# Kernel optimization log

Hardware: AMD Instinct MI355X
Metric: run time of the kernel (lower is better)

The kernel has to match this reference:

```python
import jax, jax.numpy as jnp
import numpy as np

C = 64; H = 80; W = 120; B = 2; V = 3; BV = B * V; D = 20
NEAR = 0.1; FAR = 100.0
BF16 = jnp.bfloat16


def conv2d(x, w, b, pad):
    y = jax.lax.conv_general_dilated(x, w, (1, 1), [(pad, pad), (pad, pad)],
                                     dimension_numbers=('NCHW', 'OIHW', 'NCHW'))
    return y + b[None, :, None, None]


def bn2d(x, g, b, m, v, eps=1e-5):
    # BatchNorm2d in inference mode (running stats)
    scale = g / jnp.sqrt(v + eps)
    return (x - m[None, :, None, None]) * scale[None, :, None, None] + b[None, :, None, None]


def grid_sample(feat, grid):
    # feat [N,C,Hf,Wf], grid [N,Hg,Wg,2] in [-1,1]; bilinear, zeros padding, align_corners=True
    _, _, Hf, Wf = feat.shape
    gx = (grid[..., 0] + 1.0) * 0.5 * (Wf - 1)
    gy = (grid[..., 1] + 1.0) * 0.5 * (Hf - 1)
    x0 = jnp.floor(gx); y0 = jnp.floor(gy)

    def one(f, gx, gy, x0, y0):
        def gather(xi, yi):
            valid = (xi >= 0) & (xi < Wf) & (yi >= 0) & (yi < Hf)
            xc = jnp.clip(xi, 0, Wf - 1).astype(jnp.int32)
            yc = jnp.clip(yi, 0, Hf - 1).astype(jnp.int32)
            return f[:, yc, xc] * valid.astype(f.dtype)
        wx = gx - x0; wy = gy - y0
        return (gather(x0, y0) * ((1 - wx) * (1 - wy))
                + gather(x0 + 1, y0) * (wx * (1 - wy))
                + gather(x0, y0 + 1) * ((1 - wx) * wy)
                + gather(x0 + 1, y0 + 1) * (wx * wy))
    return jax.vmap(one)(feat, gx, gy, x0, y0)


def forward(x, intrinsics, c2ws,
            pf_bn1_g, pf_bn1_b, pf_bn1_m, pf_bn1_v, pf_w1, pf_b1,
            pf_bn2_g, pf_bn2_b, pf_bn2_m, pf_bn2_v, pf_w2, pf_b2,
            cp_w, cp_b, cf_bn_g, cf_bn_b, cf_bn_m, cf_bn_v, cf_w, cf_b):
    # ---- flag[0]: predicted depth -> world xyz, position_fusion ----
    depth = 255.0 * (0.5 * jnp.tanh(x[:, 0]) + 0.5)                       # [BV,H,W]
    d16 = depth.astype(BF16)
    ug = jnp.broadcast_to(jnp.arange(W, dtype=jnp.float32)[None, :], (H, W)).astype(BF16)
    vg = jnp.broadcast_to(jnp.arange(H, dtype=jnp.float32)[:, None], (H, W)).astype(BF16)
    cam = jnp.stack([ug[None] * d16, vg[None] * d16, d16], axis=-1).reshape(BV, H * W, 3)
    Kinv = jnp.linalg.inv(intrinsics.astype(jnp.float32)).astype(BF16)
    xyz = jnp.einsum('nij,npj->npi', Kinv, cam)                           # cam coords
    xyz = jnp.einsum('nij,npj->npi', c2ws[:, :3, :3].astype(BF16), xyz) \
          + c2ws[:, :3, 3].astype(BF16)[:, None, :]                       # world coords
    xyz = xyz.reshape(BV, H, W, 3).transpose(0, 3, 1, 2).astype(x.dtype)
    h = jnp.concatenate([xyz, x], axis=1)                                 # [BV,C+3,H,W]
    h = jax.nn.silu(conv2d(bn2d(h, pf_bn1_g, pf_bn1_b, pf_bn1_m, pf_bn1_v), pf_w1, pf_b1, 4))
    h = jax.nn.silu(conv2d(bn2d(h, pf_bn2_g, pf_bn2_b, pf_bn2_m, pf_bn2_v), pf_w2, pf_b2, 4))

    # ---- flag[1]: multi-view plane-sweep correlation ----
    xr = h.reshape(B, V, C, H, W)
    vb = lambda t: t.transpose(1, 0, 2, 3, 4).reshape(BV, C, H, W)        # 'b v ... -> (v b) ...'
    feat01 = vb(xr)
    Ki = intrinsics.reshape(B, V, 3, 3)
    intr_curr = jax.lax.stop_gradient(
        (Ki * jnp.array([W, H, 1.0], jnp.float32)[None, None, :, None]).transpose(1, 0, 2, 3).reshape(BV, 3, 3))
    E = jax.lax.stop_gradient(c2ws.reshape(B, V, 4, 4))
    Einv = jnp.linalg.inv(E)
    dmin, dmax = 1.0 / FAR, 1.0 / NEAR
    depth_vals = 1.0 / (dmin + jnp.linspace(0.0, 1.0, D) * (dmax - dmin))  # [D]
    pix = jnp.stack([jnp.broadcast_to(jnp.arange(W, dtype=jnp.float32)[None, :], (H, W)),
                     jnp.broadcast_to(jnp.arange(H, dtype=jnp.float32)[:, None], (H, W)),
                     jnp.ones((H, W), jnp.float32)], 0).reshape(3, H * W)
    Kinv_c = jnp.linalg.inv(intr_curr).astype(BF16)

    corr = 0.0
    for idx in range(1, V):
        order = list(range(V))[idx:] + list(range(V))[:idx]
        feat10 = vb(xr[:, jnp.array(order)])                              # [BV,C,H,W]
        pose = jnp.concatenate([E[:, o] @ Einv[:, v0] for v0, o in enumerate(order)], axis=0)  # [BV,4,4]
        pts = jnp.einsum('bij,jp->bip', Kinv_c, pix.astype(BF16))
        pts = jnp.einsum('bij,bjp->bip', pose[:, :3, :3].astype(BF16), pts)
        pts = pts[:, :, None, :] * depth_vals.astype(BF16)[None, None, :, None] \
              + pose[:, :3, 3].astype(BF16)[:, :, None, None]             # [BV,3,D,HW]
        pts = jnp.einsum('bij,bjdp->bidp', intr_curr.astype(BF16), pts).astype(jnp.float32)
        den = jnp.maximum(pts[:, 2], 1e-3)
        grid = jnp.stack([2.0 * pts[:, 0] / den / (W - 1) - 1.0,
                          2.0 * pts[:, 1] / den / (H - 1) - 1.0], axis=-1)
        grid = jax.lax.stop_gradient(grid.reshape(BV, D * H, W, 2))
        warped = grid_sample(feat10, grid).reshape(BV, C, D, H, W)
        corr = corr + jnp.einsum('bchw,bcdhw->bdhw', feat01, warped) / (C ** 0.5)
    corr = corr / (V - 1)

    cin = jnp.concatenate([corr, feat01], axis=1)                         # [BV,D+C,H,W]
    cost = conv2d(cin, cp_w, cp_b, 1).reshape(V, B, C, H, W).transpose(1, 0, 2, 3, 4)
    fused = jnp.concatenate([cost, xr], axis=2).reshape(BV, 2 * C, H, W)
    out = jax.nn.silu(conv2d(bn2d(fused, cf_bn_g, cf_bn_b, cf_bn_m, cf_bn_v), cf_w, cf_b, 4))
    return out


def setup_inputs() -> dict:
    key = jax.random.key(0)
    ks = jax.random.split(key, 24)
    def nrm(i, shape, scale=1.0):
        return scale * jax.random.normal(ks[i], shape, jnp.float32)
    def wconv(i, shape):
        fan_in = int(np.prod(shape[1:]))
        return jax.random.normal(ks[i], shape, jnp.float32) / np.sqrt(fan_in)
    x = nrm(0, (BV, C, H, W))
    Kmat = np.tile(np.array([[1.2, 0, 0.5], [0, 1.6, 0.5], [0, 0, 1.0]], np.float32), (BV, 1, 1))
    intrinsics = jnp.asarray(Kmat)
    c2_list = []
    for i in range(BV):
        th = 0.3 * (i % V) - 0.3
        T = np.eye(4, dtype=np.float32)
        T[:3, :3] = np.array([[np.cos(th), 0, np.sin(th)], [0, 1, 0], [-np.sin(th), 0, np.cos(th)]], np.float32)
        T[:3, 3] = [0.5 * (i % V) - 0.5, 0.0, 0.1]
        c2_list.append(T)
    c2ws = jnp.asarray(np.stack(c2_list))
    # first BN sees raw world-xyz channels (magnitude ~1e4), so realistic running var there
    bn1_v = jnp.concatenate([jnp.full((3,), 1e8, jnp.float32), jnp.ones((C,), jnp.float32)])
    return dict(
        x=x, intrinsics=intrinsics, c2ws=c2ws,
        pf_bn1_g=1.0 + 0.1 * nrm(1, (C + 3,)), pf_bn1_b=0.1 * nrm(2, (C + 3,)),
        pf_bn1_m=0.1 * nrm(3, (C + 3,)), pf_bn1_v=bn1_v,
        pf_w1=wconv(4, (C, C + 3, 9, 9)), pf_b1=0.01 * nrm(5, (C,)),
        pf_bn2_g=1.0 + 0.1 * nrm(6, (C,)), pf_bn2_b=0.1 * nrm(7, (C,)),
        pf_bn2_m=0.1 * nrm(8, (C,)), pf_bn2_v=jnp.ones((C,), jnp.float32),
        pf_w2=wconv(9, (C, C, 9, 9)), pf_b2=0.01 * nrm(10, (C,)),
        cp_w=wconv(11, (C, C + D, 3, 3)), cp_b=0.01 * nrm(12, (C,)),
        cf_bn_g=1.0 + 0.1 * nrm(13, (2 * C,)), cf_bn_b=0.1 * nrm(14, (2 * C,)),
        cf_bn_m=0.1 * nrm(15, (2 * C,)), cf_bn_v=jnp.ones((2 * C,), jnp.float32),
        cf_w=wconv(16, (C, 2 * C, 9, 9)), cf_b=0.01 * nrm(17, (C,)))


def reference(x, intrinsics, c2ws,
              pf_bn1_g, pf_bn1_b, pf_bn1_m, pf_bn1_v, pf_w1, pf_b1,
              pf_bn2_g, pf_bn2_b, pf_bn2_m, pf_bn2_v, pf_w2, pf_b2,
              cp_w, cp_b, cf_bn_g, cf_bn_b, cf_bn_m, cf_bn_v, cf_w, cf_b):
    return forward(x, intrinsics, c2ws,
                   pf_bn1_g, pf_bn1_b, pf_bn1_m, pf_bn1_v, pf_w1, pf_b1,
                   pf_bn2_g, pf_bn2_b, pf_bn2_m, pf_bn2_v, pf_w2, pf_b2,
                   cp_w, cp_b, cf_bn_g, cf_bn_b, cf_bn_m, cf_bn_v, cf_w, cf_b)
```

## Files before the change

### kernel.cpp

```cpp
#include <hip/hip_runtime.h>
#include <math.h>

static constexpr int kH  = 80;
static constexpr int kW  = 120;
static constexpr int kHW = kH * kW;
static constexpr int kBV = 6;
static constexpr int kD  = 20;

typedef __attribute__((ext_vector_type(8)))  short bf16x8;
typedef __attribute__((ext_vector_type(16))) float f32x16;
typedef __attribute__((ext_vector_type(4)))  int   i32x4;
typedef __attribute__((ext_vector_type(2)))  int   i32x2;
typedef __attribute__((ext_vector_type(4)))  float float4v;

__device__ __forceinline__ float bf16r(float x) {
  unsigned u = __float_as_uint(x);
  u += 0x7FFFu + ((u >> 16) & 1u);
  return __uint_as_float(u & 0xFFFF0000u);
}
__device__ __forceinline__ unsigned short bf16c(float x) {
  unsigned u = __float_as_uint(x);
  u += 0x7FFFu + ((u >> 16) & 1u);
  return (unsigned short)(u >> 16);
}
__device__ __forceinline__ int pack2(float a, float b) {
  return (int)((unsigned)bf16c(a) | ((unsigned)bf16c(b) << 16));
}
__device__ __forceinline__ float bl(unsigned pk) {
  return __uint_as_float(pk << 16);
}
__device__ __forceinline__ float bh(unsigned pk) {
  return __uint_as_float(pk & 0xFFFF0000u);
}

struct ConstBuf {
  float bn1_s[67], bn1_o[67];
  float bn2_s[64], bn2_o[64];
  float bnf_s[128], bnf_o[128];
  float Kinv[6][9];
  float Rw[6][9];
  float tw[6][3];
  float Kinvc[6][9];
  float intrc[6][9];
  float poseR[2][6][9];
  float poseT[2][6][3];
  float dvals[20];
};

__device__ void inv3x3(const float* A, float* o) {
  float a = A[0], b = A[1], c = A[2];
  float d = A[3], e = A[4], f = A[5];
  float g = A[6], h = A[7], i = A[8];
  float det = a * (e * i - f * h) - b * (d * i - f * g) + c * (d * h - e * g);
  float id = 1.0f / det;
  o[0] = (e * i - f * h) * id;
  o[1] = -(b * i - c * h) * id;
  o[2] = (b * f - c * e) * id;
  o[3] = -(d * i - f * g) * id;
  o[4] = (a * i - c * g) * id;
  o[5] = -(a * f - c * d) * id;
  o[6] = (d * h - e * g) * id;
  o[7] = -(a * h - b * g) * id;
  o[8] = (a * e - b * d) * id;
}

__device__ void inv4x4(const float* A, float* out) {
  float M[4][8];
  for (int r = 0; r < 4; ++r) {
    for (int c = 0; c < 4; ++c) M[r][c] = A[r * 4 + c];
    for (int c = 0; c < 4; ++c) M[r][4 + c] = (r == c) ? 1.0f : 0.0f;
  }
  for (int col = 0; col < 4; ++col) {
    int p = col;
    float best = fabsf(M[col][col]);
    for (int r = col + 1; r < 4; ++r) {
      float v = fabsf(M[r][col]);
      if (v > best) { best = v; p = r; }
    }
    if (p != col)
      for (int c = 0; c < 8; ++c) { float t = M[col][c]; M[col][c] = M[p][c]; M[p][c] = t; }
    float inv = 1.0f / M[col][col];
    for (int c = 0; c < 8; ++c) M[col][c] *= inv;
    for (int r = 0; r < 4; ++r) {
      if (r == col) continue;
      float f = M[r][col];
      for (int c = 0; c < 8; ++c) M[r][c] -= f * M[col][c];
    }
  }
  for (int r = 0; r < 4; ++r)
    for (int c = 0; c < 4; ++c) out[r * 4 + c] = M[r][4 + c];
}

__device__ void mm4(const float* A, const float* B, float* C) {
  for (int r = 0; r < 4; ++r)
    for (int c = 0; c < 4; ++c) {
      float s = 0.0f;
      for (int k = 0; k < 4; ++k) s += A[r * 4 + k] * B[k * 4 + c];
      C[r * 4 + c] = s;
    }
}

__global__ void consts_kernel(const float* __restrict__ intr, const float* __restrict__ c2,
                              const float* g1, const float* b1, const float* m1, const float* v1,
                              const float* g2, const float* b2, const float* m2, const float* v2,
                              const float* gf, const float* bff, const float* mf, const float* vff,
                              ConstBuf* cb) {
  int tid = threadIdx.x;
  for (int c = tid; c < 67; c += 64) {
    float s = g1[c] / sqrtf(v1[c] + 1e-5f);
    cb->bn1_s[c] = s; cb->bn1_o[c] = b1[c] - m1[c] * s;
  }
  for (int c = tid; c < 64; c += 64) {
    float s = g2[c] / sqrtf(v2[c] + 1e-5f);
    cb->bn2_s[c] = s; cb->bn2_o[c] = b2[c] - m2[c] * s;
  }
  for (int c = tid; c < 128; c += 64) {
    float s = gf[c] / sqrtf(vff[c] + 1e-5f);
    cb->bnf_s[c] = s; cb->bnf_o[c] = bff[c] - mf[c] * s;
  }
  if (tid < 20) {
    float l = (1.0f / 19.0f) * (float)tid;
    cb->dvals[tid] = bf16r(1.0f / (0.01f + l * 9.99f));
  }
  __shared__ float Einv_s[6][16];
  if (tid < 6) {
    float Ki[9];
    inv3x3(intr + tid * 9, Ki);
    for (int k = 0; k < 9; ++k) cb->Kinv[tid][k] = bf16r(Ki[k]);
    const float* T = c2 + tid * 16;
    cb->Rw[tid][0] = bf16r(T[0]);  cb->Rw[tid][1] = bf16r(T[1]);  cb->Rw[tid][2] = bf16r(T[2]);
    cb->Rw[tid][3] = bf16r(T[4]);  cb->Rw[tid][4] = bf16r(T[5]);  cb->Rw[tid][5] = bf16r(T[6]);
    cb->Rw[tid][6] = bf16r(T[8]);  cb->Rw[tid][7] = bf16r(T[9]);  cb->Rw[tid][8] = bf16r(T[10]);
    cb->tw[tid][0] = bf16r(T[3]);  cb->tw[tid][1] = bf16r(T[7]);  cb->tw[tid][2] = bf16r(T[11]);
    inv4x4(T, Einv_s[tid]);
    int vj = tid >> 1, bj = tid & 1, ii = bj * 3 + vj;
    const float* Kk = intr + ii * 9;
    float S[9] = {Kk[0] * 120.0f, Kk[1] * 120.0f, Kk[2] * 120.0f,
                  Kk[3] * 80.0f,  Kk[4] * 80.0f,  Kk[5] * 80.0f,
                  Kk[6],          Kk[7],          Kk[8]};
    for (int k = 0; k < 9; ++k) cb->intrc[tid][k] = bf16r(S[k]);
    float Si[9];
    inv3x3(S, Si);
    for (int k = 0; k < 9; ++k) cb->Kinvc[tid][k] = bf16r(Si[k]);
  }
  __syncthreads();
  if (tid < 12) {
    int t = tid / 6, jj = tid % 6;
    int vj = jj >> 1, bj = jj & 1;
    int o = (vj + t + 1) % 3;
    float P[16];
    mm4(c2 + (bj * 3 + o) * 16, Einv_s[bj * 3 + vj], P);
    for (int r = 0; r < 3; ++r) {
      for (int c = 0; c < 3; ++c) cb->poseR[t][jj][r * 3 + c] = bf16r(P[r * 4 + c]);
      cb->poseT[t][jj][r] = bf16r(P[r * 4 + 3]);
    }
  }
}

template <int K, int CINP, int CINR>
__global__ __launch_bounds__(256)
void prep_w(const float* __restrict__ w, unsigned short* __restrict__ Wp) {
  constexpr int NCH = CINP / 32;
  constexpr int NU = K * K * NCH * 256;
  int u = blockIdx.x * 256 + threadIdx.x;
  if (u >= NU) return;
  int slot = u & 255;
  int rest = u >> 8;
  int ci = rest % NCH;
  int kk = rest / NCH;
  int ky = kk / K, kx = kk - ky * K;
  int q = slot >> 6, lu = slot & 63;
  int nt = q >> 1, kc = q & 1;
  int oc = nt * 32 + (lu & 31);
  int gi = kc * 2 + (lu >> 5);
  int chb = ci * 32 + gi * 8;
  unsigned short o[8];
#pragma unroll
  for (int e = 0; e < 8; ++e) {
    int ch = chb + e;
    float val = (ch < CINR) ? w[(((size_t)oc * CINR + ch) * K + ky) * K + kx] : 0.0f;
    o[e] = bf16c(val);
  }
  i32x4 pk;
  pk.x = (int)o[0] | ((int)o[1] << 16);
  pk.y = (int)o[2] | ((int)o[3] << 16);
  pk.z = (int)o[4] | ((int)o[5] << 16);
  pk.w = (int)o[6] | ((int)o[7] << 16);
  *(i32x4*)&Wp[(size_t)u * 8] = pk;
}

__global__ __launch_bounds__(256)
void hn_pack(const float* __restrict__ x, const ConstBuf* __restrict__ cb,
             unsigned short* __restrict__ hn_b) {
  int id = blockIdx.x * 256 + threadIdx.x;
  if (id >= kBV * kHW) return;
  int bv = id / kHW, pix = id - bv * kHW;
  int yy = pix / kW, xx = pix - yy * kW;
  float t0 = tanhf(x[(size_t)bv * 64 * kHW + pix]);
  float depth = 255.0f * (0.5f * t0 + 0.5f);
  float dz = bf16r(depth);
  float cx = bf16r((float)xx * dz);
  float cy = bf16r((float)yy * dz);
  const float* Ki = cb->Kinv[bv];
  float p0 = bf16r(Ki[0] * cx + Ki[1] * cy + Ki[2] * dz);
  float p1 = bf16r(Ki[3] * cx + Ki[4] * cy + Ki[5] * dz);
  float p2 = bf16r(Ki[6] * cx + Ki[7] * cy + Ki[8] * dz);
  const float* R = cb->Rw[bv];
  const float* tw = cb->tw[bv];
  float q[3];
  q[0] = bf16r(bf16r(R[0] * p0 + R[1] * p1 + R[2] * p2) + tw[0]);
  q[1] = bf16r(bf16r(R[3] * p0 + R[4] * p1 + R[5] * p2) + tw[1]);
  q[2] = bf16r(bf16r(R[6] * p0 + R[7] * p1 + R[8] * p2) + tw[2]);
  unsigned short* o = &hn_b[(size_t)id * 96];
  const float* xb = x + (size_t)bv * 64 * kHW + pix;
#pragma unroll
  for (int g = 0; g < 24; ++g) {
    float vv[4];
#pragma unroll
    for (int e = 0; e < 4; ++e) {
      int ch = g * 4 + e;
      float val;
      if (ch < 3) val = q[ch] * cb->bn1_s[ch] + cb->bn1_o[ch];
      else if (ch < 67) val = xb[(size_t)(ch - 3) * kHW] * cb->bn1_s[ch] + cb->bn1_o[ch];
      else val = 0.0f;
      vv[e] = val;
    }
    i32x2 pk = {pack2(vv[0], vv[1]), pack2(vv[2], vv[3])};
    *(i32x2*)(o + g * 4) = pk;
  }
}

template <int CINP, int K, int OUT>
__global__ __launch_bounds__(512)
void conv_mfma(const unsigned short* __restrict__ in_b,
               const unsigned short* __restrict__ Wp,
               const float* __restrict__ bias,
               const ConstBuf* __restrict__ cb,
               float* __restrict__ outf,
               unsigned short* __restrict__ outb,
               unsigned short* __restrict__ outb2) {
  constexpr int NCH = CINP / 32;
  constexpr int KK = K * K;
  constexpr int KH0 = (KK + 1) / 2;
  constexpr int PAD = K / 2;
  constexpr int NC = 16 + K - 1;
  constexpr int NR = 16 + K - 1;
  constexpr int NPX = NC * NR;
  __shared__ unsigned short sA[NPX * 32];

  const int tid = threadIdx.x;
  const int w = tid >> 6, l = tid & 63;
  const int mp = w >> 1, half = w & 1;
  const int bx = blockIdx.x, by = blockIdx.y, bz = blockIdx.z;
  const size_t inbase = (size_t)bz * kHW;

  const int r = l & 31, h = l >> 5;
  const int xloc = r & 15, rhi = r >> 4;
  const int kk0 = half ? KH0 : 0;
  const int myKK = half ? (KK - KH0) : KH0;
  f32x16 acc[2][2] = {};

  for (int ci = 0; ci < NCH; ++ci) {
    __syncthreads();
    for (int g2 = tid; g2 < NPX * 4; g2 += 512) {
      int px = g2 >> 2, gi = g2 & 3;
      int hy = px / NC, hx = px - hy * NC;
      int gy = by * 16 - PAD + hy, gx = bx * 16 - PAD + hx;
      bool ok = ((unsigned)gy < (unsigned)kH) && ((unsigned)gx < (unsigned)kW);
      i32x4 v = {0, 0, 0, 0};
      if (ok) v = *(const i32x4*)&in_b[(inbase + gy * kW + gx) * CINP + ci * 32 + gi * 8];
      *(i32x4*)&sA[px * 32 + ((gi ^ ((px >> 2) & 3)) << 3)] = v;
    }
    __syncthreads();

    const unsigned short* wb = Wp + ((size_t)ci * 256 + (size_t)kk0 * NCH * 256) * 8;
    const size_t kstep = (size_t)NCH * 256 * 8;
#define LOADB(dst, rdidx)                                                       \
    {                                                                           \
      const unsigned short* bp = wb + (size_t)(rdidx) * kstep + (size_t)l * 8;  \
      dst[0][0] = *(const bf16x8*)(bp);                                         \
      dst[0][1] = *(const bf16x8*)(bp + 64 * 8);                                \
      dst[1][0] = *(const bf16x8*)(bp + 128 * 8);                               \
      dst[1][1] = *(const bf16x8*)(bp + 192 * 8);                               \
    }
#define COMPUTE(rdidx, bb)                                                      \
    {                                                                           \
      const int kk = kk0 + (rdidx);                                             \
      const int ky = kk / K, kx = kk - ky * K;                                  \
      bf16x8 a[2][2];                                                           \
      _Pragma("unroll")                                                         \
      for (int m = 0; m < 2; ++m) {                                             \
        const int hp = (4 * mp + 2 * m + rhi + ky) * NC + (xloc + kx);          \
        _Pragma("unroll")                                                       \
        for (int kc = 0; kc < 2; ++kc) {                                        \
          int gi = kc * 2 + h;                                                  \
          a[m][kc] = *(const bf16x8*)&sA[hp * 32 + ((gi ^ ((hp >> 2) & 3)) << 3)]; \
        }                                                                       \
      }                                                                         \
      _Pragma("unroll")                                                         \
      for (int m = 0; m < 2; ++m)                                               \
        _Pragma("unroll")                                                       \
        for (int nt = 0; nt < 2; ++nt) {                                        \
          acc[m][nt] = __builtin_amdgcn_mfma_f32_32x32x16_bf16(a[m][0], bb[nt][0], acc[m][nt], 0, 0, 0); \
          acc[m][nt] = __builtin_amdgcn_mfma_f32_32x32x16_bf16(a[m][1], bb[nt][1], acc[m][nt], 0, 0, 0); \
        }                                                                       \
    }

    bf16x8 b0[2][2], b1[2][2];
    LOADB(b0, 0);
    int rd = 0;
    for (; rd + 2 <= myKK; rd += 2) {
      LOADB(b1, rd + 1);
      COMPUTE(rd, b0);
      if (rd + 2 < myKK) LOADB(b0, rd + 2);
      COMPUTE(rd + 1, b1);
    }
    if (rd < myKK) COMPUTE(rd, b0);
#undef LOADB
#undef COMPUTE
  }

  float* scratch = (float*)sA;
#pragma unroll
  for (int cm = 0; cm < 2; ++cm) {
#pragma unroll
    for (int cn = 0; cn < 2; ++cn) {
      float* sp = scratch + ((mp * 64 + l) * 16);
      __syncthreads();
      if (half == 1) {
#pragma unroll
        for (int q = 0; q < 16; ++q) sp[q] = acc[cm][cn][q];
      }
      __syncthreads();
      if (half == 0) {
#pragma unroll
        for (int q = 0; q < 16; ++q) acc[cm][cn][q] += sp[q];
      }
    }
  }
  if (half == 1) return;

#pragma unroll
  for (int m = 0; m < 2; ++m) {
#pragma unroll
    for (int nt = 0; nt < 2; ++nt) {
      const int oc = nt * 32 + (l & 31);
      const float bs = bias[oc];
      float s2 = 0.f, o2 = 0.f;
      if (OUT == 0) { s2 = cb->bn2_s[oc]; o2 = cb->bn2_o[oc]; }
      if (OUT == 1) { s2 = cb->bnf_s[64 + oc]; o2 = cb->bnf_o[64 + oc]; }
      if (OUT == 2) { s2 = cb->bnf_s[oc]; o2 = cb->bnf_o[oc]; }
#pragma unroll
      for (int reg = 0; reg < 16; ++reg) {
        int row = (reg & 3) + 8 * (reg >> 2) + 4 * h;
        int x = bx * 16 + (row & 15);
        if (x >= kW) continue;
        int y = by * 16 + 4 * mp + 2 * m + (row >> 4);
        float v = acc[m][nt][reg] + bs;
        if (OUT != 2) v = v / (1.0f + expf(-v));
        if (OUT == 0) {
          size_t px = inbase + y * kW + x;
          outb[px * 64 + oc] = bf16c(v * s2 + o2);
        } else if (OUT == 1) {
          size_t px = inbase + y * kW + x;
          outb[px * 64 + oc] = bf16c(v);
          outb2[px * 128 + 64 + oc] = bf16c(v * s2 + o2);
        } else if (OUT == 2) {
          int i = (bz & 1) * 3 + (bz >> 1);
          size_t px = (size_t)i * kHW + y * kW + x;
          outb[px * 128 + oc] = bf16c(v * s2 + o2);
        } else {
          outf[((size_t)bz * 64 + oc) * kHW + y * kW + x] = v;
        }
      }
    }
  }
}

__global__ __launch_bounds__(256)
void corr_kernel(const unsigned short* __restrict__ h_b, const ConstBuf* __restrict__ cb,
                 unsigned short* __restrict__ cin_b) {
  __shared__ float sgeo[4][2][40][8];
  const int tid = threadIdx.x;
  const int w = tid >> 6, lane = tid & 63;
  const int pair = blockIdx.x * 4 + w;
  const int j = pair / (kHW / 2);
  const int pix = (pair - j * (kHW / 2)) * 2;
  const int b = j & 1, v = j >> 1;
  const int ph = lane >> 5, cl = lane & 31;
  const int pixl = pix + ph;
  const int dst = b * 3 + v;
  const unsigned f01pk =
      ((const unsigned*)(h_b + ((size_t)dst * kHW + pixl) * 64))[cl];
  const float f01lo = bl(f01pk), f01hi = bh(f01pk);
  const char* sb0 = (const char*)(h_b + (size_t)(b * 3 + ((v + 1) % 3)) * kHW * 64);
  const char* sb1 = (const char*)(h_b + (size_t)(b * 3 + ((v + 2) % 3)) * kHW * 64);

  for (int job = lane; job < 80; job += 64) {
    const int p = job / 40, jj = job - p * 40;
    const int d = jj >> 1, t = jj & 1;
    const int pp = pix + p;
    const int yyp = pp / kW, xxp = pp - yyp * kW;
    const float* Kc = cb->Kinvc[j];
    const float* IC = cb->intrc[j];
    const float uf = (float)xxp, vf = (float)yyp;
    float p1_0 = bf16r(Kc[0] * uf + Kc[1] * vf + Kc[2]);
    float p1_1 = bf16r(Kc[3] * uf + Kc[4] * vf + Kc[5]);
    float p1_2 = bf16r(Kc[6] * uf + Kc[7] * vf + Kc[8]);
    const float* PR = cb->poseR[t][j];
    const float* PT = cb->poseT[t][j];
    float p20 = bf16r(PR[0] * p1_0 + PR[1] * p1_1 + PR[2] * p1_2);
    float p21 = bf16r(PR[3] * p1_0 + PR[4] * p1_1 + PR[5] * p1_2);
    float p22 = bf16r(PR[6] * p1_0 + PR[7] * p1_1 + PR[8] * p1_2);
    float dv = cb->dvals[d];
    float q0 = bf16r(bf16r(p20 * dv) + PT[0]);
    float q1 = bf16r(bf16r(p21 * dv) + PT[1]);
    float q2 = bf16r(bf16r(p22 * dv) + PT[2]);
    float s0 = bf16r(IC[0] * q0 + IC[1] * q1 + IC[2] * q2);
    float s1 = bf16r(IC[3] * q0 + IC[4] * q1 + IC[5] * q2);
    float s2 = bf16r(IC[6] * q0 + IC[7] * q1 + IC[8] * q2);
    float den = fmaxf(s2, 1e-3f);
    float g0 = 2.0f * s0 / den / 119.0f - 1.0f;
    float g1 = 2.0f * s1 / den / 79.0f - 1.0f;
    float gx = (g0 + 1.0f) * 0.5f * 119.0f;
    float gy = (g1 + 1.0f) * 0.5f * 79.0f;
    float x0f = floorf(gx), y0f = floorf(gy);
    float wx = gx - x0f, wy = gy - y0f;
    float x1f = x0f + 1.0f, y1f = y0f + 1.0f;
    float vx0 = (x0f >= 0.0f && x0f < 120.0f) ? 1.0f : 0.0f;
    float vx1 = (x1f >= 0.0f && x1f < 120.0f) ? 1.0f : 0.0f;
    float vy0 = (y0f >= 0.0f && y0f < 80.0f) ? 1.0f : 0.0f;
    float vy1 = (y1f >= 0.0f && y1f < 80.0f) ? 1.0f : 0.0f;
    int xi0 = (int)fminf(fmaxf(x0f, 0.0f), 119.0f);
    int xi1 = (int)fminf(fmaxf(x1f, 0.0f), 119.0f);
    int yi0 = (int)fminf(fmaxf(y0f, 0.0f), 79.0f);
    int yi1 = (int)fminf(fmaxf(y1f, 0.0f), 79.0f);
    int r0b = yi0 * (kW * 128), r1b = yi1 * (kW * 128);
    int c0b = xi0 * 128, c1b = xi1 * 128;
    float* gp = sgeo[w][p][jj];
    gp[0] = __int_as_float(r0b + c0b);
    gp[1] = __int_as_float(r0b + c1b);
    gp[2] = __int_as_float(r1b + c0b);
    gp[3] = __int_as_float(r1b + c1b);
    gp[4] = ((1.0f - wx) * (1.0f - wy)) * (vx0 * vy0);
    gp[5] = (wx * (1.0f - wy)) * (vx1 * vy0);
    gp[6] = ((1.0f - wx) * wy) * (vx0 * vy1);
    gp[7] = (wx * wy) * (vx1 * vy1);
  }
  __syncthreads();

  unsigned short* op = &cin_b[(size_t)(j * kHW + pixl) * 96];
  *(unsigned*)(op + 20 + 2 * cl) = f01pk;
  if (cl < 6) *(unsigned*)(op + 84 + 2 * cl) = 0u;

  const unsigned cl4 = (unsigned)cl * 4u;
#pragma unroll 2
  for (int d = 0; d < kD; ++d) {
    float a = 0.0f;
#pragma unroll
    for (int t = 0; t < 2; ++t) {
      const char* sb = t ? sb1 : sb0;
      const float* gp = sgeo[w][ph][d * 2 + t];
      float4v ga = *(const float4v*)gp;
      float4v gb = *(const float4v*)(gp + 4);
      unsigned k00 = *(const unsigned*)(sb + ((unsigned)__float_as_int(ga.x) + cl4));
      unsigned k10 = *(const unsigned*)(sb + ((unsigned)__float_as_int(ga.y) + cl4));
      unsigned k01 = *(const unsigned*)(sb + ((unsigned)__float_as_int(ga.z) + cl4));
      unsigned k11 = *(const unsigned*)(sb + ((unsigned)__float_as_int(ga.w) + cl4));
      float al = gb.x * bl(k00) + gb.y * bl(k10) + gb.z * bl(k01) + gb.w * bl(k11);
      float ah = gb.x * bh(k00) + gb.y * bh(k10) + gb.z * bh(k01) + gb.w * bh(k11);
      a += al * f01lo + ah * f01hi;
    }
#pragma unroll
    for (int off = 16; off > 0; off >>= 1) a += __shfl_xor(a, off, 64);
    if (cl == 0) op[d] = bf16c(a * 0.0625f);
  }
}

extern "C" void kernel_launch(void* const* d_in, const int* in_sizes, int n_in,
                              void* d_out, int out_size, void* d_ws, size_t ws_size,
                              hipStream_t stream) {
  (void)in_sizes; (void)n_in; (void)out_size; (void)ws_size;
  const float* x    = (const float*)d_in[0];
  const float* intr = (const float*)d_in[1];
  const float* c2w  = (const float*)d_in[2];
  const float* bn1g = (const float*)d_in[3];
  const float* bn1b = (const float*)d_in[4];
  const float* bn1m = (const float*)d_in[5];
  const float* bn1v = (const float*)d_in[6];
  const float* w1   = (const float*)d_in[7];
  const float* b1   = (const float*)d_in[8];
  const float* bn2g = (const float*)d_in[9];
  const float* bn2b = (const float*)d_in[10];
  const float* bn2m = (const float*)d_in[11];
  const float* bn2v = (const float*)d_in[12];
  const float* w2   = (const float*)d_in[13];
  const float* b2   = (const float*)d_in[14];
  const float* cpw  = (const float*)d_in[15];
  const float* cpb  = (const float*)d_in[16];
  const float* bnfg = (const float*)d_in[17];
  const float* bnfb = (const float*)d_in[18];
  const float* bnfm = (const float*)d_in[19];
  const float* bnfv = (const float*)d_in[20];
  const float* wf   = (const float*)d_in[21];
  const float* bff  = (const float*)d_in[22];

  char* ws = (char*)d_ws;
  ConstBuf* cb            = (ConstBuf*)ws;
  unsigned short* hn_b    = (unsigned short*)(ws + 8192);
  unsigned short* h1_b    = (unsigned short*)(ws + 11067392);
  unsigned short* h_b     = (unsigned short*)(ws + 18440192);
  unsigned short* cin_b   = (unsigned short*)(ws + 33185792);
  unsigned short* fused_b = (unsigned short*)(ws + 44244992);
  unsigned short* Wp1     = (unsigned short*)(ws + 58990592);
  unsigned short* Wp2     = (unsigned short*)(ws + 59985920);
  unsigned short* Wpc     = (unsigned short*)(ws + 60649472);
  unsigned short* Wpf     = (unsigned short*)(ws + 60760064);

  consts_kernel<<<1, 64, 0, stream>>>(intr, c2w, bn1g, bn1b, bn1m, bn1v,
                                      bn2g, bn2b, bn2m, bn2v, bnfg, bnfb, bnfm, bnfv, cb);
  prep_w<9, 96, 67><<<243, 256, 0, stream>>>(w1, Wp1);
  prep_w<9, 64, 64><<<162, 256, 0, stream>>>(w2, Wp2);
  prep_w<3, 96, 84><<<27, 256, 0, stream>>>(cpw, Wpc);
  prep_w<9, 128, 128><<<324, 256, 0, stream>>>(wf, Wpf);
  hn_pack<<<225, 256, 0, stream>>>(x, cb, hn_b);

  dim3 cgrid(8, 5, 6);
  conv_mfma<96, 9, 0><<<cgrid, 512, 0, stream>>>(hn_b, Wp1, b1, cb, nullptr, h1_b, nullptr);
  conv_mfma<64, 9, 1><<<cgrid, 512, 0, stream>>>(h1_b, Wp2, b2, cb, nullptr, h_b, fused_b);
  corr_kernel<<<7200, 256, 0, stream>>>(h_b, cb, cin_b);
  conv_mfma<96, 3, 2><<<cgrid, 512, 0, stream>>>(cin_b, Wpc, cpb, cb, nullptr, fused_b, nullptr);
  conv_mfma<128, 9, 3><<<cgrid, 512, 0, stream>>>(fused_b, Wpf, bff, cb, (float*)d_out, nullptr, nullptr);
}
```

Baseline: 334.0 us.

## Halve conv tile height and split output channels across waves

Each conv block now covers 16x8 output pixels instead of 16x16, and the grid doubles in y to compensate. The eight waves are remapped so each handles one m-pair and one 32-channel half of the outputs, giving half the accumulators and B-fragment loads per wave. The aim is more blocks (480 vs 240) for better CU occupancy and fewer registers per wave. The cost is a larger share of halo pixels loaded per output and weight fragments re-read by more waves.

```diff
diff --git a/kernel.cpp b/kernel.cpp
--- a/kernel.cpp
+++ b/kernel.cpp
@@ -244,13 +244,14 @@
   constexpr int KH0 = (KK + 1) / 2;
   constexpr int PAD = K / 2;
   constexpr int NC = 16 + K - 1;
-  constexpr int NR = 16 + K - 1;
+  constexpr int NR = 8 + K - 1;
   constexpr int NPX = NC * NR;
-  __shared__ unsigned short sA[NPX * 32];
+  constexpr int SAW = (NPX * 32 > 8192) ? NPX * 32 : 8192;
+  __shared__ unsigned short sA[SAW];
 
   const int tid = threadIdx.x;
   const int w = tid >> 6, l = tid & 63;
-  const int mp = w >> 1, half = w & 1;
+  const int mp = w & 1, ntq = (w >> 1) & 1, half = w >> 2;
   const int bx = blockIdx.x, by = blockIdx.y, bz = blockIdx.z;
   const size_t inbase = (size_t)bz * kHW;
 
@@ -258,14 +259,14 @@
   const int xloc = r & 15, rhi = r >> 4;
   const int kk0 = half ? KH0 : 0;
   const int myKK = half ? (KK - KH0) : KH0;
-  f32x16 acc[2][2] = {};
+  f32x16 acc[2] = {};
 
   for (int ci = 0; ci < NCH; ++ci) {
     __syncthreads();
     for (int g2 = tid; g2 < NPX * 4; g2 += 512) {
       int px = g2 >> 2, gi = g2 & 3;
       int hy = px / NC, hx = px - hy * NC;
-      int gy = by * 16 - PAD + hy, gx = bx * 16 - PAD + hx;
+      int gy = by * 8 - PAD + hy, gx = bx * 16 - PAD + hx;
       bool ok = ((unsigned)gy < (unsigned)kH) && ((unsigned)gx < (unsigned)kW);
       i32x4 v = {0, 0, 0, 0};
       if (ok) v = *(const i32x4*)&in_b[(inbase + gy * kW + gx) * CINP + ci * 32 + gi * 8];
@@ -277,11 +278,10 @@
     const size_t kstep = (size_t)NCH * 256 * 8;
 #define LOADB(dst, rdidx)                                                       \
     {                                                                           \
-      const unsigned short* bp = wb + (size_t)(rdidx) * kstep + (size_t)l * 8;  \
-      dst[0][0] = *(const bf16x8*)(bp);                                         \
-      dst[0][1] = *(const bf16x8*)(bp + 64 * 8);                                \
-      dst[1][0] = *(const bf16x8*)(bp + 128 * 8);                               \
-      dst[1][1] = *(const bf16x8*)(bp + 192 * 8);                               \
+      const unsigned short* bp =                                                \
+          wb + (size_t)(rdidx) * kstep + (size_t)(ntq * 128 + l) * 8;           \
+      dst[0] = *(const bf16x8*)(bp);                                            \
+      dst[1] = *(const bf16x8*)(bp + 64 * 8);                                   \
     }
 #define COMPUTE(rdidx, bb)                                                      \
     {                                                                           \
@@ -298,15 +298,13 @@
         }                                                                       \
       }                                                                         \
       _Pragma("unroll")                                                         \
-      for (int m = 0; m < 2; ++m)                                               \
-        _Pragma("unroll")                                                       \
-        for (int nt = 0; nt < 2; ++nt) {                                        \
-          acc[m][nt] = __builtin_amdgcn_mfma_f32_32x32x16_bf16(a[m][0], bb[nt][0], acc[m][nt], 0, 0, 0); \
-          acc[m][nt] = __builtin_amdgcn_mfma_f32_32x32x16_bf16(a[m][1], bb[nt][1], acc[m][nt], 0, 0, 0); \
-        }                                                                       \
-    }
-
-    bf16x8 b0[2][2], b1[2][2];
+      for (int m = 0; m < 2; ++m) {                                             \
+        acc[m] = __builtin_amdgcn_mfma_f32_32x32x16_bf16(a[m][0], bb[0], acc[m], 0, 0, 0); \
+        acc[m] = __builtin_amdgcn_mfma_f32_32x32x16_bf16(a[m][1], bb[1], acc[m], 0, 0, 0); \
+      }                                                                         \
+    }
+
+    bf16x8 b0[2], b1[2];
     LOADB(b0, 0);
     int rd = 0;
     for (; rd + 2 <= myKK; rd += 2) {
@@ -323,55 +321,49 @@
   float* scratch = (float*)sA;
 #pragma unroll
   for (int cm = 0; cm < 2; ++cm) {
-#pragma unroll
-    for (int cn = 0; cn < 2; ++cn) {
-      float* sp = scratch + ((mp * 64 + l) * 16);
-      __syncthreads();
-      if (half == 1) {
-#pragma unroll
-        for (int q = 0; q < 16; ++q) sp[q] = acc[cm][cn][q];
-      }
-      __syncthreads();
-      if (half == 0) {
-#pragma unroll
-        for (int q = 0; q < 16; ++q) acc[cm][cn][q] += sp[q];
-      }
+    float* sp = scratch + (((w & 3) * 64 + l) * 16);
+    __syncthreads();
+    if (half == 1) {
+#pragma unroll
+      for (int q = 0; q < 16; ++q) sp[q] = acc[cm][q];
+    }
+    __syncthreads();
+    if (half == 0) {
+#pragma unroll
+      for (int q = 0; q < 16; ++q) acc[cm][q] += sp[q];
     }
   }
   if (half == 1) return;
 
 #pragma unroll
   for (int m = 0; m < 2; ++m) {
-#pragma unroll
-    for (int nt = 0; nt < 2; ++nt) {
-      const int oc = nt * 32 + (l & 31);
-      const float bs = bias[oc];
-      float s2 = 0.f, o2 = 0.f;
-      if (OUT == 0) { s2 = cb->bn2_s[oc]; o2 = cb->bn2_o[oc]; }
-      if (OUT == 1) { s2 = cb->bnf_s[64 + oc]; o2 = cb->bnf_o[64 + oc]; }
-      if (OUT == 2) { s2 = cb->bnf_s[oc]; o2 = cb->bnf_o[oc]; }
-#pragma unroll
-      for (int reg = 0; reg < 16; ++reg) {
-        int row = (reg & 3) + 8 * (reg >> 2) + 4 * h;
-        int x = bx * 16 + (row & 15);
-        if (x >= kW) continue;
-        int y = by * 16 + 4 * mp + 2 * m + (row >> 4);
-        float v = acc[m][nt][reg] + bs;
-        if (OUT != 2) v = v / (1.0f + expf(-v));
-        if (OUT == 0) {
-          size_t px = inbase + y * kW + x;
-          outb[px * 64 + oc] = bf16c(v * s2 + o2);
-        } else if (OUT == 1) {
-          size_t px = inbase + y * kW + x;
-          outb[px * 64 + oc] = bf16c(v);
-          outb2[px * 128 + 64 + oc] = bf16c(v * s2 + o2);
-        } else if (OUT == 2) {
-          int i = (bz & 1) * 3 + (bz >> 1);
-          size_t px = (size_t)i * kHW + y * kW + x;
-          outb[px * 128 + oc] = bf16c(v * s2 + o2);
-        } else {
-          outf[((size_t)bz * 64 + oc) * kHW + y * kW + x] = v;
-        }
+    const int oc = ntq * 32 + (l & 31);
+    const float bs = bias[oc];
+    float s2 = 0.f, o2 = 0.f;
+    if (OUT == 0) { s2 = cb->bn2_s[oc]; o2 = cb->bn2_o[oc]; }
+    if (OUT == 1) { s2 = cb->bnf_s[64 + oc]; o2 = cb->bnf_o[64 + oc]; }
+    if (OUT == 2) { s2 = cb->bnf_s[oc]; o2 = cb->bnf_o[oc]; }
+#pragma unroll
+    for (int reg = 0; reg < 16; ++reg) {
+      int row = (reg & 3) + 8 * (reg >> 2) + 4 * h;
+      int x = bx * 16 + (row & 15);
+      if (x >= kW) continue;
+      int y = by * 8 + 4 * mp + 2 * m + (row >> 4);
+      float v = acc[m][reg] + bs;
+      if (OUT != 2) v = v / (1.0f + expf(-v));
+      if (OUT == 0) {
+        size_t px = inbase + y * kW + x;
+        outb[px * 64 + oc] = bf16c(v * s2 + o2);
+      } else if (OUT == 1) {
+        size_t px = inbase + y * kW + x;
+        outb[px * 64 + oc] = bf16c(v);
+        outb2[px * 128 + 64 + oc] = bf16c(v * s2 + o2);
+      } else if (OUT == 2) {
+        int i = (bz & 1) * 3 + (bz >> 1);
+        size_t px = (size_t)i * kHW + y * kW + x;
+        outb[px * 128 + oc] = bf16c(v * s2 + o2);
+      } else {
+        outf[((size_t)bz * 64 + oc) * kHW + y * kW + x] = v;
       }
     }
   }
@@ -525,7 +517,7 @@
   prep_w<9, 128, 128><<<324, 256, 0, stream>>>(wf, Wpf);
   hn_pack<<<225, 256, 0, stream>>>(x, cb, hn_b);
 
-  dim3 cgrid(8, 5, 6);
+  dim3 cgrid(8, 10, 6);
   conv_mfma<96, 9, 0><<<cgrid, 512, 0, stream>>>(hn_b, Wp1, b1, cb, nullptr, h1_b, nullptr);
   conv_mfma<64, 9, 1><<<cgrid, 512, 0, stream>>>(h1_b, Wp2, b2, cb, nullptr, h_b, fused_b);
   corr_kernel<<<7200, 256, 0, stream>>>(h_b, cb, cin_b);
```

After: 337.4 us. Within noise of the previous version (+1.0%).
